# Optimization experiments

Measured on AMD Instinct MI355X. Metric: run time of the kernel, lower is better.

## Reference

```python
import jax, jax.numpy as jnp
import numpy as np

B, N, D = 2, 256, 128
LN_EPS = 1e-5


def _linear_params(key, d, scale):
    kw, kb = jax.random.split(key)
    W = jax.random.normal(kw, (d, d), jnp.float32) * scale
    b = jax.random.normal(kb, (d,), jnp.float32) * 0.02
    return W, b


def setup_inputs() -> dict:
    key = jax.random.key(0)
    ks = jax.random.split(key, 8)
    hidden_states = jax.random.normal(ks[0], (B, N, D), jnp.float32)
    structure_matrix = jax.random.normal(ks[1], (B, N, N, D), jnp.float32)
    scale = 1.0 / np.sqrt(D).astype(np.float32)
    Wq, bq = _linear_params(ks[2], D, scale)
    Wk, bk = _linear_params(ks[3], D, scale)
    Wv, bv = _linear_params(ks[4], D, scale)
    Wo, bo = _linear_params(ks[5], D, scale)
    ln_g = jnp.ones((D,), jnp.float32)
    ln_b = jnp.zeros((D,), jnp.float32)
    return dict(hidden_states=hidden_states, structure_matrix=structure_matrix,
                Wq=Wq, bq=bq, Wk=Wk, bk=bk, Wv=Wv, bv=bv, Wo=Wo, bo=bo,
                ln_g=ln_g, ln_b=ln_b)


def reference(hidden_states, structure_matrix, Wq, bq, Wk, bk, Wv, bv, Wo, bo, ln_g, ln_b):
    # hidden_states is accepted by the original forward but never used.
    d = structure_matrix.shape[-1]
    q = structure_matrix @ Wq + bq  # [B,N,N,D]
    k = structure_matrix @ Wk + bk
    v = structure_matrix @ Wv + bv
    # scores[b,i,j,k] = <Q[b,i,k,:], K[b,i,j,:]> / sqrt(D)
    # (equivalent to the torch broadcast multiply+sum, expressed as batched GEMM)
    scores = jnp.einsum('bikd,bijd->bijk', q, k) / jnp.sqrt(jnp.asarray(d, scores_dtype := q.dtype))
    probs = jax.nn.relu(scores)  # dropout is identity in eval mode
    # context[b,i,j,d] = sum_k probs[b,i,j,k] * V[b,i,k,d]
    ctx = jnp.einsum('bijk,bikd->bijd', probs, v)
    out = ctx @ Wo + bo
    x = out + structure_matrix  # residual
    mu = jnp.mean(x, axis=-1, keepdims=True)
    var = jnp.var(x, axis=-1, keepdims=True)
    return (x - mu) * jax.lax.rsqrt(var + LN_EPS) * ln_g + ln_b
```

## Files before the change

### kernel.cpp

```cpp
#include <hip/hip_runtime.h>

#define DEV static __device__ __forceinline__

typedef __bf16 bf16x8 __attribute__((ext_vector_type(8)));
typedef float  f32x16 __attribute__((ext_vector_type(16)));

DEV int rowmap(int r, int hi) { return (r & 3) + 8 * (r >> 2) + 4 * hi; }

DEV int swz128(int row, int col) {
  return row * 256 + (((((col >> 3) ^ (row & 7)) << 3) | (col & 7)) << 1);
}
DEV int swzVT(int d, int k) {
  return d * 512 + (((((k >> 3) ^ (d & 7)) << 3) | (k & 7)) << 1);
}

DEV unsigned pack2(float lo, float hi) {
  union { __bf16 h[2]; unsigned u; } x;
  x.h[0] = (__bf16)lo; x.h[1] = (__bf16)hi;
  return x.u;
}

DEV bf16x8 mk_frag(float d0, float d1, float d2, float d3,
                   float d4, float d5, float d6, float d7, int lane) {
  unsigned a0 = pack2(d0, d1), a1 = pack2(d2, d3);
  unsigned b0 = pack2(d4, d5), b1 = pack2(d6, d7);
  unsigned a0s = __shfl_xor(a0, 32), a1s = __shfl_xor(a1, 32);
  unsigned b0s = __shfl_xor(b0, 32), b1s = __shfl_xor(b1, 32);
  bool lo = lane < 32;
  union { unsigned u[4]; bf16x8 v; } r;
  r.u[0] = lo ? a0  : b0s;
  r.u[1] = lo ? a1  : b1s;
  r.u[2] = lo ? a0s : b0;
  r.u[3] = lo ? a1s : b1;
  return r.v;
}

DEV f32x16 fzero() {
  f32x16 z;
  #pragma unroll
  for (int i = 0; i < 16; ++i) z[i] = 0.f;
  return z;
}

DEV void stage_w(const float* __restrict__ W, char* WT, int tid) {
  #pragma unroll
  for (int it = 0; it < 32; ++it) {
    int idx = tid + it * 512;
    int e = idx >> 7, dp = idx & 127;
    *reinterpret_cast<__bf16*>(WT + swz128(dp, e)) = (__bf16)W[idx];
  }
}

DEV void proj32(const bf16x8 sf[8], const char* WT, int ml, int hi, f32x16 acc[4]) {
  #pragma unroll
  for (int t = 0; t < 4; ++t) acc[t] = fzero();
  #pragma unroll
  for (int kk = 0; kk < 8; ++kk) {
    #pragma unroll
    for (int t = 0; t < 4; ++t) {
      bf16x8 wf = *reinterpret_cast<const bf16x8*>(
          WT + swz128(32 * t + ml, 16 * kk + 8 * hi));
      acc[t] = __builtin_amdgcn_mfma_f32_32x32x16_bf16(sf[kk], wf, acc[t], 0, 0, 0);
    }
  }
}

__global__ __launch_bounds__(512, 2)
void sapd_fused(const float* __restrict__ S,
                const float* __restrict__ Wq, const float* __restrict__ bq,
                const float* __restrict__ Wk, const float* __restrict__ bk,
                const float* __restrict__ Wv, const float* __restrict__ bv,
                const float* __restrict__ Wo, const float* __restrict__ bo,
                const float* __restrict__ lg, const float* __restrict__ lb,
                float* __restrict__ out)
{
  extern __shared__ char smem[];
  char* QL = smem;
  char* VT = smem + 65536;
  char* WT = smem + 131072;

  const int tid  = threadIdx.x;
  const int lane = tid & 63;
  const int w    = tid >> 6;
  const int ml   = lane & 31;
  const int hi   = lane >> 5;
  const int bi   = blockIdx.x;
  const size_t sbase = (size_t)bi * (256 * 128);

  bf16x8 sfrag[8];
  {
    const float* srow = S + sbase + (size_t)(32 * w + ml) * 128;
    #pragma unroll
    for (int kk = 0; kk < 8; ++kk) {
      float4 a = *reinterpret_cast<const float4*>(srow + 16 * kk + 8 * hi);
      float4 b = *reinterpret_cast<const float4*>(srow + 16 * kk + 8 * hi + 4);
      bf16x8 f;
      f[0] = (__bf16)a.x; f[1] = (__bf16)a.y; f[2] = (__bf16)a.z; f[3] = (__bf16)a.w;
      f[4] = (__bf16)b.x; f[5] = (__bf16)b.y; f[6] = (__bf16)b.z; f[7] = (__bf16)b.w;
      sfrag[kk] = f;
    }
  }

  f32x16 acc[4];

  stage_w(Wk, WT, tid);
  __syncthreads();
  proj32(sfrag, WT, ml, hi, acc);
  {
    char* KS = VT + w * 8192;
    #pragma unroll
    for (int t = 0; t < 4; ++t) {
      float bb = bk[32 * t + ml];
      #pragma unroll
      for (int r = 0; r < 16; ++r)
        *reinterpret_cast<__bf16*>(KS + swz128(rowmap(r, hi), 32 * t + ml)) =
            (__bf16)(acc[t][r] + bb);
    }
  }
  __syncthreads();
  bf16x8 kfrag[8];
  {
    const char* KS = VT + w * 8192;
    #pragma unroll
    for (int kk = 0; kk < 8; ++kk)
      kfrag[kk] = *reinterpret_cast<const bf16x8*>(
          KS + swz128(ml, 16 * kk + 8 * hi));
  }
  __syncthreads();

  stage_w(Wv, WT, tid);
  __syncthreads();
  proj32(sfrag, WT, ml, hi, acc);
  #pragma unroll
  for (int t = 0; t < 4; ++t) {
    float bb = bv[32 * t + ml];
    int d = 32 * t + ml;
    #pragma unroll
    for (int p = 0; p < 8; ++p) {
      int k = 32 * w + rowmap(2 * p, hi);
      *reinterpret_cast<unsigned*>(VT + swzVT(d, k)) =
          pack2(acc[t][2 * p] + bb, acc[t][2 * p + 1] + bb);
    }
  }
  __syncthreads();

  stage_w(Wq, WT, tid);
  __syncthreads();
  proj32(sfrag, WT, ml, hi, acc);
  #pragma unroll
  for (int t = 0; t < 4; ++t) {
    float bb = bq[32 * t + ml];
    #pragma unroll
    for (int r = 0; r < 16; ++r)
      *reinterpret_cast<__bf16*>(
          QL + swz128(32 * w + rowmap(r, hi), 32 * t + ml)) =
          (__bf16)(acc[t][r] + bb);
  }
  __syncthreads();
  stage_w(Wo, WT, tid);
  __syncthreads();

  f32x16 ctx[4];
  #pragma unroll
  for (int m = 0; m < 4; ++m) ctx[m] = fzero();
  const float SC = 0.088388347648318447f;

  #pragma unroll 2
  for (int kt = 0; kt < 8; ++kt) {
    f32x16 sa = fzero();
    #pragma unroll
    for (int kk = 0; kk < 8; ++kk) {
      bf16x8 qf = *reinterpret_cast<const bf16x8*>(
          QL + swz128(32 * kt + ml, 16 * kk + 8 * hi));
      sa = __builtin_amdgcn_mfma_f32_32x32x16_bf16(qf, kfrag[kk], sa, 0, 0, 0);
    }
    float p[16];
    #pragma unroll
    for (int r = 0; r < 16; ++r) p[r] = fmaxf(sa[r] * SC, 0.f);
    bf16x8 pf0 = mk_frag(p[0], p[1], p[2], p[3], p[4], p[5], p[6], p[7], lane);
    bf16x8 pf1 = mk_frag(p[8], p[9], p[10], p[11], p[12], p[13], p[14], p[15], lane);
    #pragma unroll
    for (int m = 0; m < 4; ++m) {
      bf16x8 vf0 = *reinterpret_cast<const bf16x8*>(
          VT + swzVT(32 * m + ml, 32 * kt + 8 * hi));
      ctx[m] = __builtin_amdgcn_mfma_f32_32x32x16_bf16(vf0, pf0, ctx[m], 0, 0, 0);
      bf16x8 vf1 = *reinterpret_cast<const bf16x8*>(
          VT + swzVT(32 * m + ml, 32 * kt + 16 + 8 * hi));
      ctx[m] = __builtin_amdgcn_mfma_f32_32x32x16_bf16(vf1, pf1, ctx[m], 0, 0, 0);
    }
  }

  bf16x8 cf[8];
  #pragma unroll
  for (int m = 0; m < 4; ++m) {
    cf[2 * m]     = mk_frag(ctx[m][0], ctx[m][1], ctx[m][2], ctx[m][3],
                            ctx[m][4], ctx[m][5], ctx[m][6], ctx[m][7], lane);
    cf[2 * m + 1] = mk_frag(ctx[m][8], ctx[m][9], ctx[m][10], ctx[m][11],
                            ctx[m][12], ctx[m][13], ctx[m][14], ctx[m][15], lane);
  }
  f32x16 oa[4];
  #pragma unroll
  for (int t = 0; t < 4; ++t) oa[t] = fzero();
  #pragma unroll
  for (int kk = 0; kk < 8; ++kk) {
    #pragma unroll
    for (int t = 0; t < 4; ++t) {
      bf16x8 wf = *reinterpret_cast<const bf16x8*>(
          WT + swz128(32 * t + ml, 16 * kk + 8 * hi));
      oa[t] = __builtin_amdgcn_mfma_f32_32x32x16_bf16(cf[kk], wf, oa[t], 0, 0, 0);
    }
  }

  float gg[4], lbv[4], bov[4];
  #pragma unroll
  for (int t = 0; t < 4; ++t) {
    gg[t]  = lg[32 * t + ml];
    lbv[t] = lb[32 * t + ml];
    bov[t] = bo[32 * t + ml];
  }
  float sum[16], ssq[16];
  #pragma unroll
  for (int r = 0; r < 16; ++r) { sum[r] = 0.f; ssq[r] = 0.f; }
  #pragma unroll
  for (int t = 0; t < 4; ++t) {
    #pragma unroll
    for (int r = 0; r < 16; ++r) {
      size_t off = sbase + (size_t)(32 * w + rowmap(r, hi)) * 128 + 32 * t + ml;
      float x = oa[t][r] + bov[t] + S[off];
      oa[t][r] = x;
      sum[r] += x;
      ssq[r] += x * x;
    }
  }
  #pragma unroll
  for (int r = 0; r < 16; ++r) {
    float s_ = sum[r], q_ = ssq[r];
    #pragma unroll
    for (int m = 1; m <= 16; m <<= 1) {
      s_ += __shfl_xor(s_, m);
      q_ += __shfl_xor(q_, m);
    }
    float mu = s_ * (1.f / 128.f);
    float var = q_ * (1.f / 128.f) - mu * mu;
    float rs = rsqrtf(var + 1e-5f);
    float* orow = out + sbase + (size_t)(32 * w + rowmap(r, hi)) * 128;
    #pragma unroll
    for (int t = 0; t < 4; ++t)
      orow[32 * t + ml] = (oa[t][r] - mu) * rs * gg[t] + lbv[t];
  }
}

extern "C" void kernel_launch(void* const* d_in, const int* in_sizes, int n_in,
                              void* d_out, int out_size, void* d_ws, size_t ws_size,
                              hipStream_t stream) {
  (void)in_sizes; (void)n_in; (void)d_ws; (void)ws_size; (void)out_size;
  const float* S  = (const float*)d_in[1];
  const float* Wq = (const float*)d_in[2];
  const float* bq = (const float*)d_in[3];
  const float* Wk = (const float*)d_in[4];
  const float* bk = (const float*)d_in[5];
  const float* Wv = (const float*)d_in[6];
  const float* bv = (const float*)d_in[7];
  const float* Wo = (const float*)d_in[8];
  const float* bo = (const float*)d_in[9];
  const float* lg = (const float*)d_in[10];
  const float* lb = (const float*)d_in[11];
  float* out = (float*)d_out;

  constexpr int SMEM = 163840;
  (void)hipFuncSetAttribute((const void*)sapd_fused,
                            hipFuncAttributeMaxDynamicSharedMemorySize, SMEM);
  sapd_fused<<<dim3(512), dim3(512), SMEM, stream>>>(
      S, Wq, bq, Wk, bk, Wv, bv, Wo, bo, lg, lb, out);
}
```

Baseline: 71.94 us.

## Pre-convert weights to swizzled bf16 in workspace and reorganize LDS staging

```diff
diff --git a/kernel.cpp b/kernel.cpp
--- a/kernel.cpp
+++ b/kernel.cpp
@@ -7,11 +7,11 @@
 
 DEV int rowmap(int r, int hi) { return (r & 3) + 8 * (r >> 2) + 4 * hi; }
 
-DEV int swz128(int row, int col) {
-  return row * 256 + (((((col >> 3) ^ (row & 7)) << 3) | (col & 7)) << 1);
-}
-DEV int swzVT(int d, int k) {
-  return d * 512 + (((((k >> 3) ^ (d & 7)) << 3) | (k & 7)) << 1);
+DEV int swzQ(int row, int col) {
+  return row * 256 + (((((col >> 3) ^ (row & 15)) << 3) | (col & 7)) << 1);
+}
+DEV int swzV(int d, int k) {
+  return d * 512 + (((((k >> 3) ^ (d & 31)) << 3) | (k & 7)) << 1);
 }
 
 DEV unsigned pack2(float lo, float hi) {
@@ -42,16 +42,21 @@
   return z;
 }
 
-DEV void stage_w(const float* __restrict__ W, char* WT, int tid) {
+DEV void copy_lds(char* dst, const char* src, int bytes, int tid) {
+  for (int off = tid * 16; off < bytes; off += 512 * 16)
+    *reinterpret_cast<int4*>(dst + off) = *reinterpret_cast<const int4*>(src + off);
+}
+
+DEV void stage_w32(const float* __restrict__ W, char* dst, int tid) {
   #pragma unroll
   for (int it = 0; it < 32; ++it) {
     int idx = tid + it * 512;
     int e = idx >> 7, dp = idx & 127;
-    *reinterpret_cast<__bf16*>(WT + swz128(dp, e)) = (__bf16)W[idx];
-  }
-}
-
-DEV void proj32(const bf16x8 sf[8], const char* WT, int ml, int hi, f32x16 acc[4]) {
+    *reinterpret_cast<__bf16*>(dst + swzQ(dp, e)) = (__bf16)W[idx];
+  }
+}
+
+DEV void proj32(const bf16x8 sf[8], const char* Wt, int ml, int hi, f32x16 acc[4]) {
   #pragma unroll
   for (int t = 0; t < 4; ++t) acc[t] = fzero();
   #pragma unroll
@@ -59,33 +64,44 @@
     #pragma unroll
     for (int t = 0; t < 4; ++t) {
       bf16x8 wf = *reinterpret_cast<const bf16x8*>(
-          WT + swz128(32 * t + ml, 16 * kk + 8 * hi));
+          Wt + swzQ(32 * t + ml, 16 * kk + 8 * hi));
       acc[t] = __builtin_amdgcn_mfma_f32_32x32x16_bf16(sf[kk], wf, acc[t], 0, 0, 0);
     }
   }
 }
 
+__global__ void prep_wt(const float* __restrict__ Wk, const float* __restrict__ Wq,
+                        const float* __restrict__ Wv, const float* __restrict__ Wo,
+                        __bf16* __restrict__ wt) {
+  int idx = blockIdx.x * 256 + threadIdx.x;
+  const float* W[4] = {Wk, Wq, Wv, Wo};
+  int m = idx >> 14, rem = idx & 16383;
+  int e = rem >> 7, dp = rem & 127;
+  wt[m * 16384 + (swzQ(dp, e) >> 1)] = (__bf16)W[m][rem];
+}
+
+template<bool WS>
 __global__ __launch_bounds__(512, 2)
 void sapd_fused(const float* __restrict__ S,
-                const float* __restrict__ Wq, const float* __restrict__ bq,
-                const float* __restrict__ Wk, const float* __restrict__ bk,
-                const float* __restrict__ Wv, const float* __restrict__ bv,
-                const float* __restrict__ Wo, const float* __restrict__ bo,
+                const float* __restrict__ bq, const float* __restrict__ bk,
+                const float* __restrict__ bv, const float* __restrict__ bo,
+                const float* __restrict__ Wq, const float* __restrict__ Wk,
+                const float* __restrict__ Wv, const float* __restrict__ Wo,
                 const float* __restrict__ lg, const float* __restrict__ lb,
+                const __bf16* __restrict__ wt,
                 float* __restrict__ out)
 {
   extern __shared__ char smem[];
   char* QL = smem;
   char* VT = smem + 65536;
-  char* WT = smem + 131072;
 
   const int tid  = threadIdx.x;
   const int lane = tid & 63;
   const int w    = tid >> 6;
   const int ml   = lane & 31;
   const int hi   = lane >> 5;
-  const int bi   = blockIdx.x;
-  const size_t sbase = (size_t)bi * (256 * 128);
+  const size_t sbase = (size_t)blockIdx.x * (256 * 128);
+  const char* wsc = (const char*)wt;
 
   bf16x8 sfrag[8];
   {
@@ -101,36 +117,48 @@
     }
   }
 
+  if (WS) {
+    copy_lds(VT, wsc, 65536, tid);
+  } else {
+    stage_w32(Wk, VT, tid);
+    stage_w32(Wq, VT + 32768, tid);
+  }
+  __syncthreads();
+
   f32x16 acc[4];
-
-  stage_w(Wk, WT, tid);
-  __syncthreads();
-  proj32(sfrag, WT, ml, hi, acc);
-  {
-    char* KS = VT + w * 8192;
-    #pragma unroll
-    for (int t = 0; t < 4; ++t) {
-      float bb = bk[32 * t + ml];
-      #pragma unroll
-      for (int r = 0; r < 16; ++r)
-        *reinterpret_cast<__bf16*>(KS + swz128(rowmap(r, hi), 32 * t + ml)) =
-            (__bf16)(acc[t][r] + bb);
-    }
-  }
-  __syncthreads();
+  char* KS = QL + w * 8192;
+
+  proj32(sfrag, VT, ml, hi, acc);
+  #pragma unroll
+  for (int t = 0; t < 4; ++t) {
+    float bb = bk[32 * t + ml];
+    #pragma unroll
+    for (int r = 0; r < 16; ++r)
+      *reinterpret_cast<__bf16*>(KS + swzQ(rowmap(r, hi), 32 * t + ml)) =
+          (__bf16)(acc[t][r] + bb);
+  }
   bf16x8 kfrag[8];
-  {
-    const char* KS = VT + w * 8192;
-    #pragma unroll
-    for (int kk = 0; kk < 8; ++kk)
-      kfrag[kk] = *reinterpret_cast<const bf16x8*>(
-          KS + swz128(ml, 16 * kk + 8 * hi));
-  }
-  __syncthreads();
-
-  stage_w(Wv, WT, tid);
-  __syncthreads();
-  proj32(sfrag, WT, ml, hi, acc);
+  #pragma unroll
+  for (int kk = 0; kk < 8; ++kk)
+    kfrag[kk] = *reinterpret_cast<const bf16x8*>(KS + swzQ(ml, 16 * kk + 8 * hi));
+
+  proj32(sfrag, VT + 32768, ml, hi, acc);
+  #pragma unroll
+  for (int t = 0; t < 4; ++t) {
+    float bb = bq[32 * t + ml];
+    #pragma unroll
+    for (int r = 0; r < 16; ++r)
+      *reinterpret_cast<__bf16*>(KS + swzQ(rowmap(r, hi), 32 * t + ml)) =
+          (__bf16)(acc[t][r] + bb);
+  }
+  __syncthreads();
+
+  if (WS) copy_lds(VT, wsc + 65536, 32768, tid);
+  else    stage_w32(Wv, VT, tid);
+  __syncthreads();
+
+  proj32(sfrag, VT, ml, hi, acc);
+  __syncthreads();
   #pragma unroll
   for (int t = 0; t < 4; ++t) {
     float bb = bv[32 * t + ml];
@@ -138,26 +166,10 @@
     #pragma unroll
     for (int p = 0; p < 8; ++p) {
       int k = 32 * w + rowmap(2 * p, hi);
-      *reinterpret_cast<unsigned*>(VT + swzVT(d, k)) =
+      *reinterpret_cast<unsigned*>(VT + swzV(d, k)) =
           pack2(acc[t][2 * p] + bb, acc[t][2 * p + 1] + bb);
     }
   }
-  __syncthreads();
-
-  stage_w(Wq, WT, tid);
-  __syncthreads();
-  proj32(sfrag, WT, ml, hi, acc);
-  #pragma unroll
-  for (int t = 0; t < 4; ++t) {
-    float bb = bq[32 * t + ml];
-    #pragma unroll
-    for (int r = 0; r < 16; ++r)
-      *reinterpret_cast<__bf16*>(
-          QL + swz128(32 * w + rowmap(r, hi), 32 * t + ml)) =
-          (__bf16)(acc[t][r] + bb);
-  }
-  __syncthreads();
-  stage_w(Wo, WT, tid);
   __syncthreads();
 
   f32x16 ctx[4];
@@ -171,7 +183,7 @@
     #pragma unroll
     for (int kk = 0; kk < 8; ++kk) {
       bf16x8 qf = *reinterpret_cast<const bf16x8*>(
-          QL + swz128(32 * kt + ml, 16 * kk + 8 * hi));
+          QL + swzQ(32 * kt + ml, 16 * kk + 8 * hi));
       sa = __builtin_amdgcn_mfma_f32_32x32x16_bf16(qf, kfrag[kk], sa, 0, 0, 0);
     }
     float p[16];
@@ -182,10 +194,10 @@
     #pragma unroll
     for (int m = 0; m < 4; ++m) {
       bf16x8 vf0 = *reinterpret_cast<const bf16x8*>(
-          VT + swzVT(32 * m + ml, 32 * kt + 8 * hi));
+          VT + swzV(32 * m + ml, 32 * kt + 8 * hi));
       ctx[m] = __builtin_amdgcn_mfma_f32_32x32x16_bf16(vf0, pf0, ctx[m], 0, 0, 0);
       bf16x8 vf1 = *reinterpret_cast<const bf16x8*>(
-          VT + swzVT(32 * m + ml, 32 * kt + 16 + 8 * hi));
+          VT + swzV(32 * m + ml, 32 * kt + 16 + 8 * hi));
       ctx[m] = __builtin_amdgcn_mfma_f32_32x32x16_bf16(vf1, pf1, ctx[m], 0, 0, 0);
     }
   }
@@ -198,6 +210,11 @@
     cf[2 * m + 1] = mk_frag(ctx[m][8], ctx[m][9], ctx[m][10], ctx[m][11],
                             ctx[m][12], ctx[m][13], ctx[m][14], ctx[m][15], lane);
   }
+  __syncthreads();
+  if (WS) copy_lds(QL, wsc + 98304, 32768, tid);
+  else    stage_w32(Wo, QL, tid);
+  __syncthreads();
+
   f32x16 oa[4];
   #pragma unroll
   for (int t = 0; t < 4; ++t) oa[t] = fzero();
@@ -206,7 +223,7 @@
     #pragma unroll
     for (int t = 0; t < 4; ++t) {
       bf16x8 wf = *reinterpret_cast<const bf16x8*>(
-          WT + swz128(32 * t + ml, 16 * kk + 8 * hi));
+          QL + swzQ(32 * t + ml, 16 * kk + 8 * hi));
       oa[t] = __builtin_amdgcn_mfma_f32_32x32x16_bf16(cf[kk], wf, oa[t], 0, 0, 0);
     }
   }
@@ -253,7 +270,7 @@
 extern "C" void kernel_launch(void* const* d_in, const int* in_sizes, int n_in,
                               void* d_out, int out_size, void* d_ws, size_t ws_size,
                               hipStream_t stream) {
-  (void)in_sizes; (void)n_in; (void)d_ws; (void)ws_size; (void)out_size;
+  (void)in_sizes; (void)n_in; (void)out_size;
   const float* S  = (const float*)d_in[1];
   const float* Wq = (const float*)d_in[2];
   const float* bq = (const float*)d_in[3];
@@ -267,9 +284,18 @@
   const float* lb = (const float*)d_in[11];
   float* out = (float*)d_out;
 
-  constexpr int SMEM = 163840;
-  (void)hipFuncSetAttribute((const void*)sapd_fused,
-                            hipFuncAttributeMaxDynamicSharedMemorySize, SMEM);
-  sapd_fused<<<dim3(512), dim3(512), SMEM, stream>>>(
-      S, Wq, bq, Wk, bk, Wv, bv, Wo, bo, lg, lb, out);
-}
+  constexpr int SMEM = 131072;
+  bool use_ws = (d_ws != nullptr) && (ws_size >= 131072);
+  if (use_ws) {
+    prep_wt<<<dim3(256), dim3(256), 0, stream>>>(Wk, Wq, Wv, Wo, (__bf16*)d_ws);
+    (void)hipFuncSetAttribute(reinterpret_cast<const void*>(&sapd_fused<true>),
+                              hipFuncAttributeMaxDynamicSharedMemorySize, SMEM);
+    sapd_fused<true><<<dim3(512), dim3(512), SMEM, stream>>>(
+        S, bq, bk, bv, bo, Wq, Wk, Wv, Wo, lg, lb, (const __bf16*)d_ws, out);
+  } else {
+    (void)hipFuncSetAttribute(reinterpret_cast<const void*>(&sapd_fused<false>),
+                              hipFuncAttributeMaxDynamicSharedMemorySize, SMEM);
+    sapd_fused<false><<<dim3(512), dim3(512), SMEM, stream>>>(
+        S, bq, bk, bv, bo, Wq, Wk, Wv, Wo, lg, lb, nullptr, out);
+  }
+}
```

New measurement: 69.34 us. 1.04x faster.
